# Optimization experiments

Hardware: AMD Instinct MI355X
Metric: run time of the kernel (lower is better)

Reference implementation:

```python
import jax, jax.numpy as jnp
import numpy as np

EMBED_TIME = 128
NUM_HEADS = 4
INPUT_DIM = 64
NHIDDEN = 256
B, LQ, LK = 4, 256, 512


def setup_inputs() -> dict:
    key = jax.random.key(0)
    ks = jax.random.split(key, 8)
    scale = np.float32(0.05)
    return {
        "query": jax.random.normal(ks[0], (B, LQ, EMBED_TIME), jnp.float32),
        "key_ts": jax.random.normal(ks[1], (B, LK, EMBED_TIME), jnp.float32),
        "value": jax.random.normal(ks[2], (B, LK, INPUT_DIM), jnp.float32),
        "mask": jax.random.randint(ks[3], (B, LK, INPUT_DIM), 0, 2, jnp.int32),
        # params stored [in, out] (transpose of torch nn.Linear convention)
        "Wq": jax.random.normal(ks[4], (EMBED_TIME, EMBED_TIME), jnp.float32) * scale,
        "bq": jnp.zeros((EMBED_TIME,), jnp.float32),
        "Wk": jax.random.normal(ks[5], (EMBED_TIME, EMBED_TIME), jnp.float32) * scale,
        "bk": jnp.zeros((EMBED_TIME,), jnp.float32),
        "W3": jax.random.normal(ks[6], (INPUT_DIM * NUM_HEADS, NHIDDEN), jnp.float32) * scale,
        "b3": jnp.zeros((NHIDDEN,), jnp.float32),
    }


def reference(query, key_ts, value, mask, Wq, bq, Wk, bk, W3, b3):
    b, lk, d = value.shape  # B, Lk, input_dim
    h = NUM_HEADS
    dk = EMBED_TIME // h
    # project & split heads: [B, L, E] -> [B, h, L, dk]
    q = (query @ Wq + bq).reshape(b, -1, h, dk).transpose(0, 2, 1, 3)
    k = (key_ts @ Wk + bk).reshape(b, -1, h, dk).transpose(0, 2, 1, 3)
    # scaled dot-product time scores: [B, h, Lq, Lk]
    scores = jnp.einsum('bhqe,bhke->bhqk', q, k) / np.float32(np.sqrt(dk))
    # broadcast scores over value feature dim, mask per feature: [B, h, Lq, Lk, D]
    scores = jnp.where(mask[:, None, None, :, :] == 0, jnp.float32(-1e9), scores[..., None])
    # softmax over key (time) axis, per feature
    p_attn = jax.nn.softmax(scores, axis=-2)
    # elementwise weighted reduce over Lk: [B, h, Lq, D]
    x = jnp.einsum('bhqkd,bkd->bhqd', p_attn, value)
    x = x.transpose(0, 2, 1, 3).reshape(b, -1, h * d)  # [B, Lq, h*D]
    # replicate reinitialize_dim: permute input columns of last layer by descending L1 norm
    perm = jnp.argsort(-jnp.sum(jnp.abs(W3), axis=1))
    return x @ W3[perm] + b3
```

## Files before the change

### kernel.cpp

```cpp
#include <hip/hip_runtime.h>
#include <math.h>

#define ETIME 128
#define NHEADS 4
#define DK 32
#define DIN 64
#define NHID 256
#define BB 4
#define LQg 256
#define LKg 512
#define KC 128
#define KCN 4
#define QT 16

__global__ __launch_bounds__(256) void proj_kernel(
    const float* __restrict__ query, const float* __restrict__ key_ts,
    const float* __restrict__ Wq, const float* __restrict__ bq,
    const float* __restrict__ Wk, const float* __restrict__ bk,
    float* __restrict__ qbuf, float* __restrict__ kbuf)
{
    __shared__ float in_lds[8][ETIME];
    const int t = threadIdx.x;
    const int r0 = blockIdx.x * 8;
    const bool is_q = (r0 < BB * LQg);
    const float* in   = is_q ? (query + (size_t)r0 * ETIME)
                             : (key_ts + (size_t)(r0 - BB * LQg) * ETIME);
    const float* W    = is_q ? Wq : Wk;
    const float* bias = is_q ? bq : bk;
    float* outp       = is_q ? (qbuf + (size_t)r0 * ETIME)
                             : (kbuf + (size_t)(r0 - BB * LQg) * ETIME);

    reinterpret_cast<float4*>(&in_lds[0][0])[t] =
        reinterpret_cast<const float4*>(in)[t];
    __syncthreads();

    const int j4 = t & 31;
    const int row = t >> 5;
    const float4* W4 = reinterpret_cast<const float4*>(W);
    float4 acc = make_float4(0.f, 0.f, 0.f, 0.f);
#pragma unroll 8
    for (int i = 0; i < ETIME; ++i) {
        const float4 w = W4[i * 32 + j4];
        const float xv = in_lds[row][i];
        acc.x = fmaf(xv, w.x, acc.x);
        acc.y = fmaf(xv, w.y, acc.y);
        acc.z = fmaf(xv, w.z, acc.z);
        acc.w = fmaf(xv, w.w, acc.w);
    }
    const float4 bb = reinterpret_cast<const float4*>(bias)[j4];
    acc.x += bb.x; acc.y += bb.y; acc.z += bb.z; acc.w += bb.w;
    reinterpret_cast<float4*>(outp + row * ETIME)[j4] = acc;
}

__global__ __launch_bounds__(256) void prep_kernel(
    const float* __restrict__ value, const int* __restrict__ mask,
    const float* __restrict__ W3,
    float2* __restrict__ vmbuf, float* __restrict__ sbuf)
{
    const int t = threadIdx.x;
    if (blockIdx.x < 256) {
        const int i = blockIdx.x * 256 + t;
        for (int idx = i; idx < BB * LKg * DIN; idx += 256 * 256) {
            const float mf = (float)mask[idx];
            vmbuf[idx] = make_float2(mf, value[idx] * mf);
        }
    } else {
        __shared__ float red[4];
        const int row = blockIdx.x - 256;
        float a = fabsf(W3[(size_t)row * NHID + t]);
#pragma unroll
        for (int off = 32; off; off >>= 1) a += __shfl_xor(a, off, 64);
        if ((t & 63) == 0) red[t >> 6] = a;
        __syncthreads();
        if (t == 0) sbuf[row] = red[0] + red[1] + red[2] + red[3];
    }
}

__global__ __launch_bounds__(NHID) void rank_kernel(
    const float* __restrict__ sbuf, int* __restrict__ perm)
{
    __shared__ float s[NHID];
    const int t = threadIdx.x;
    s[t] = sbuf[t];
    __syncthreads();
    const float si = s[t];
    int rank = 0;
#pragma unroll 8
    for (int j = 0; j < NHID; ++j) {
        const float sj = s[j];
        rank += (sj > si) || (sj == si && j < t);
    }
    perm[rank] = t;
}

__global__ __launch_bounds__(256, 4) void attn_chunk(
    const float* __restrict__ qbuf, const float* __restrict__ kbuf,
    const float2* __restrict__ vmbuf, float2* __restrict__ pbuf)
{
    __shared__ float qlds[QT][DK];
    __shared__ float klds[KC][DK + 1];
    __shared__ float S[QT][KC];

    const int t = threadIdx.x;
    int bid = blockIdx.x;
    bid = (bid & 7) * 128 + (bid >> 3);
    const int kc = bid & 3;
    const int qt = (bid >> 2) & 15;
    const int h  = (bid >> 6) & 3;
    const int b  = bid >> 8;
    const int qbase = qt * QT;
    const int kbase = kc * KC;

    for (int e = t; e < QT * DK; e += 256) {
        int q = e >> 5, i = e & 31;
        qlds[q][i] = qbuf[(size_t)(b * LQg + qbase + q) * ETIME + h * DK + i];
    }
    for (int e = t; e < KC * DK; e += 256) {
        int k = e >> 5, i = e & 31;
        klds[k][i] = kbuf[(size_t)(b * LKg + kbase + k) * ETIME + h * DK + i];
    }
    __syncthreads();

    {
        const int k = t & 127;
        const int qg = t >> 7;
        float acc[8] = {0, 0, 0, 0, 0, 0, 0, 0};
        for (int i = 0; i < DK; ++i) {
            float kv = klds[k][i];
#pragma unroll
            for (int jj = 0; jj < 8; ++jj)
                acc[jj] = fmaf(qlds[qg * 8 + jj][i], kv, acc[jj]);
        }
        const float rsq = 0.17677669529663687f;
#pragma unroll
        for (int jj = 0; jj < 8; ++jj)
            S[qg * 8 + jj][k] = __expf(acc[jj] * rsq);
    }
    __syncthreads();

    {
        const int d = t & 63;
        const int w = t >> 6;
        float num[4] = {0, 0, 0, 0}, den[4] = {0, 0, 0, 0};
        const float2* vp = vmbuf + (size_t)(b * LKg + kbase) * DIN + d;
#pragma unroll 4
        for (int k = 0; k < KC; ++k) {
            const float2 vm = vp[(size_t)k * DIN];
#pragma unroll
            for (int jj = 0; jj < 4; ++jj) {
                const float e = S[w * 4 + jj][k];
                num[jj] = fmaf(e, vm.y, num[jj]);
                den[jj] = fmaf(e, vm.x, den[jj]);
            }
        }
#pragma unroll
        for (int jj = 0; jj < 4; ++jj) {
            const int q = qbase + w * 4 + jj;
            pbuf[((size_t)((b * NHEADS + h) * LQg + q) * KCN + kc) * DIN + d] =
                make_float2(den[jj], num[jj]);
        }
    }
}

__global__ __launch_bounds__(256) void combine_kernel(
    const float2* __restrict__ pbuf, const int* __restrict__ perm,
    float* __restrict__ x2)
{
    const int t = threadIdx.x;
    const int bid = blockIdx.x;
    const int qt = bid & 15, h = (bid >> 4) & 3, b = bid >> 6;
    const int d = t & 63, w = t >> 6;
    const int pc = perm[h * DIN + d];
#pragma unroll
    for (int jj = 0; jj < 4; ++jj) {
        const int q = qt * QT + w * 4 + jj;
        const float2* pp = pbuf + ((size_t)((b * NHEADS + h) * LQg + q) * KCN) * DIN + d;
        float num = 0.f, den = 0.f;
#pragma unroll
        for (int kc = 0; kc < KCN; ++kc) {
            const float2 v = pp[kc * DIN];
            den += v.x; num += v.y;
        }
        x2[(size_t)(b * LQg + q) * NHID + pc] = num / den;
    }
}

__global__ __launch_bounds__(256) void out_kernel(
    const float* __restrict__ x2, const float* __restrict__ W3,
    const float* __restrict__ b3, float* __restrict__ out)
{
    __shared__ float x_lds[4][NHID];
    const int n = threadIdx.x;
    const int r0 = blockIdx.x * 4;
    reinterpret_cast<float4*>(&x_lds[0][0])[n] =
        reinterpret_cast<const float4*>(x2 + (size_t)r0 * NHID)[n];
    __syncthreads();

    float acc[4] = {0, 0, 0, 0};
#pragma unroll 8
    for (int c = 0; c < NHID; ++c) {
        const float w = W3[(size_t)c * NHID + n];
#pragma unroll
        for (int r = 0; r < 4; ++r) acc[r] = fmaf(x_lds[r][c], w, acc[r]);
    }
    const float bn = b3[n];
#pragma unroll
    for (int r = 0; r < 4; ++r) out[(size_t)(r0 + r) * NHID + n] = acc[r] + bn;
}

extern "C" void kernel_launch(void* const* d_in, const int* in_sizes, int n_in,
                              void* d_out, int out_size, void* d_ws, size_t ws_size,
                              hipStream_t stream) {
    const float* query  = (const float*)d_in[0];
    const float* key_ts = (const float*)d_in[1];
    const float* value  = (const float*)d_in[2];
    const int*   mask   = (const int*)d_in[3];
    const float* Wq     = (const float*)d_in[4];
    const float* bq     = (const float*)d_in[5];
    const float* Wk     = (const float*)d_in[6];
    const float* bk     = (const float*)d_in[7];
    const float* W3     = (const float*)d_in[8];
    const float* b3     = (const float*)d_in[9];
    float* out = (float*)d_out;

    char* ws = (char*)d_ws;
    float*  qbuf  = (float*) (ws);
    float*  kbuf  = (float*) (ws + (512u  << 10));
    float2* vmbuf = (float2*)(ws + (1536u << 10));
    float*  x2buf = (float*) (ws + (2560u << 10));
    float2* pbuf  = (float2*)(ws + (3584u << 10));
    int*    perm  = (int*)   (ws + (11776u << 10));
    float*  sbuf  = (float*) (ws + (11780u << 10));

    proj_kernel<<<384, 256, 0, stream>>>(query, key_ts, Wq, bq, Wk, bk, qbuf, kbuf);
    prep_kernel<<<512, 256, 0, stream>>>(value, mask, W3, vmbuf, sbuf);
    rank_kernel<<<1, NHID, 0, stream>>>(sbuf, perm);
    attn_chunk<<<BB * NHEADS * QT * KCN, 256, 0, stream>>>(qbuf, kbuf, vmbuf, pbuf);
    combine_kernel<<<BB * NHEADS * (LQg / QT), 256, 0, stream>>>(pbuf, perm, x2buf);
    out_kernel<<<BB * LQg / 4, 256, 0, stream>>>(x2buf, W3, b3, out);
}
```

Baseline: 56.97 us.

## Fuse prep, rank, combine and output kernels; vectorize attention loads

Merges projection, value/mask prep and W3 norm computation into one launch, and folds the rank computation and partial-sum combine into the output GEMM kernel, cutting the pipeline from six launches to three. The attention kernel now reads K rows directly into registers as float4, prescales Q, and uses float4 LDS reads in both inner loops. The cost is that every output block recomputes the 256-element rank and re-reads sbuf, and register pressure in the attention kernel goes up.

```diff
diff --git a/kernel.cpp b/kernel.cpp
--- a/kernel.cpp
+++ b/kernel.cpp
@@ -13,60 +13,58 @@
 #define KCN 4
 #define QT 16
 
-__global__ __launch_bounds__(256) void proj_kernel(
+__global__ __launch_bounds__(256) void prep_all(
     const float* __restrict__ query, const float* __restrict__ key_ts,
     const float* __restrict__ Wq, const float* __restrict__ bq,
     const float* __restrict__ Wk, const float* __restrict__ bk,
-    float* __restrict__ qbuf, float* __restrict__ kbuf)
+    const float* __restrict__ value, const int* __restrict__ mask,
+    const float* __restrict__ W3,
+    float* __restrict__ qbuf, float* __restrict__ kbuf,
+    float2* __restrict__ vmbuf, float* __restrict__ sbuf)
 {
     __shared__ float in_lds[8][ETIME];
+    __shared__ float red[4];
     const int t = threadIdx.x;
-    const int r0 = blockIdx.x * 8;
-    const bool is_q = (r0 < BB * LQg);
-    const float* in   = is_q ? (query + (size_t)r0 * ETIME)
-                             : (key_ts + (size_t)(r0 - BB * LQg) * ETIME);
-    const float* W    = is_q ? Wq : Wk;
-    const float* bias = is_q ? bq : bk;
-    float* outp       = is_q ? (qbuf + (size_t)r0 * ETIME)
-                             : (kbuf + (size_t)(r0 - BB * LQg) * ETIME);
-
-    reinterpret_cast<float4*>(&in_lds[0][0])[t] =
-        reinterpret_cast<const float4*>(in)[t];
-    __syncthreads();
-
-    const int j4 = t & 31;
-    const int row = t >> 5;
-    const float4* W4 = reinterpret_cast<const float4*>(W);
-    float4 acc = make_float4(0.f, 0.f, 0.f, 0.f);
+    const int blk = blockIdx.x;
+
+    if (blk < 384) {
+        const int r0 = blk * 8;
+        const bool is_q = (r0 < BB * LQg);
+        const float* in   = is_q ? (query + (size_t)r0 * ETIME)
+                                 : (key_ts + (size_t)(r0 - BB * LQg) * ETIME);
+        const float* W    = is_q ? Wq : Wk;
+        const float* bias = is_q ? bq : bk;
+        float* outp       = is_q ? (qbuf + (size_t)r0 * ETIME)
+                                 : (kbuf + (size_t)(r0 - BB * LQg) * ETIME);
+
+        reinterpret_cast<float4*>(&in_lds[0][0])[t] =
+            reinterpret_cast<const float4*>(in)[t];
+        __syncthreads();
+
+        const int j4 = t & 31;
+        const int row = t >> 5;
+        const float4* W4 = reinterpret_cast<const float4*>(W);
+        float4 acc = make_float4(0.f, 0.f, 0.f, 0.f);
 #pragma unroll 8
-    for (int i = 0; i < ETIME; ++i) {
-        const float4 w = W4[i * 32 + j4];
-        const float xv = in_lds[row][i];
-        acc.x = fmaf(xv, w.x, acc.x);
-        acc.y = fmaf(xv, w.y, acc.y);
-        acc.z = fmaf(xv, w.z, acc.z);
-        acc.w = fmaf(xv, w.w, acc.w);
-    }
-    const float4 bb = reinterpret_cast<const float4*>(bias)[j4];
-    acc.x += bb.x; acc.y += bb.y; acc.z += bb.z; acc.w += bb.w;
-    reinterpret_cast<float4*>(outp + row * ETIME)[j4] = acc;
-}
-
-__global__ __launch_bounds__(256) void prep_kernel(
-    const float* __restrict__ value, const int* __restrict__ mask,
-    const float* __restrict__ W3,
-    float2* __restrict__ vmbuf, float* __restrict__ sbuf)
-{
-    const int t = threadIdx.x;
-    if (blockIdx.x < 256) {
-        const int i = blockIdx.x * 256 + t;
+        for (int i = 0; i < ETIME; ++i) {
+            const float4 w = W4[i * 32 + j4];
+            const float xv = in_lds[row][i];
+            acc.x = fmaf(xv, w.x, acc.x);
+            acc.y = fmaf(xv, w.y, acc.y);
+            acc.z = fmaf(xv, w.z, acc.z);
+            acc.w = fmaf(xv, w.w, acc.w);
+        }
+        const float4 bb = reinterpret_cast<const float4*>(bias)[j4];
+        acc.x += bb.x; acc.y += bb.y; acc.z += bb.z; acc.w += bb.w;
+        reinterpret_cast<float4*>(outp + row * ETIME)[j4] = acc;
+    } else if (blk < 640) {
+        const int i = (blk - 384) * 256 + t;
         for (int idx = i; idx < BB * LKg * DIN; idx += 256 * 256) {
             const float mf = (float)mask[idx];
             vmbuf[idx] = make_float2(mf, value[idx] * mf);
         }
     } else {
-        __shared__ float red[4];
-        const int row = blockIdx.x - 256;
+        const int row = blk - 640;
         float a = fabsf(W3[(size_t)row * NHID + t]);
 #pragma unroll
         for (int off = 32; off; off >>= 1) a += __shfl_xor(a, off, 64);
@@ -74,23 +72,6 @@
         __syncthreads();
         if (t == 0) sbuf[row] = red[0] + red[1] + red[2] + red[3];
     }
-}
-
-__global__ __launch_bounds__(NHID) void rank_kernel(
-    const float* __restrict__ sbuf, int* __restrict__ perm)
-{
-    __shared__ float s[NHID];
-    const int t = threadIdx.x;
-    s[t] = sbuf[t];
-    __syncthreads();
-    const float si = s[t];
-    int rank = 0;
-#pragma unroll 8
-    for (int j = 0; j < NHID; ++j) {
-        const float sj = s[j];
-        rank += (sj > si) || (sj == si && j < t);
-    }
-    perm[rank] = t;
 }
 
 __global__ __launch_bounds__(256, 4) void attn_chunk(
@@ -98,7 +79,6 @@
     const float2* __restrict__ vmbuf, float2* __restrict__ pbuf)
 {
     __shared__ float qlds[QT][DK];
-    __shared__ float klds[KC][DK + 1];
     __shared__ float S[QT][KC];
 
     const int t = threadIdx.x;
@@ -111,30 +91,41 @@
     const int qbase = qt * QT;
     const int kbase = kc * KC;
 
-    for (int e = t; e < QT * DK; e += 256) {
-        int q = e >> 5, i = e & 31;
-        qlds[q][i] = qbuf[(size_t)(b * LQg + qbase + q) * ETIME + h * DK + i];
-    }
-    for (int e = t; e < KC * DK; e += 256) {
-        int k = e >> 5, i = e & 31;
-        klds[k][i] = kbuf[(size_t)(b * LKg + kbase + k) * ETIME + h * DK + i];
+    if (t < 128) {
+        const int q = t >> 3, j = t & 7;
+        float4 v = reinterpret_cast<const float4*>(
+            qbuf + (size_t)(b * LQg + qbase + q) * ETIME + h * DK)[j];
+        const float rsq = 0.17677669529663687f;
+        v.x *= rsq; v.y *= rsq; v.z *= rsq; v.w *= rsq;
+        reinterpret_cast<float4*>(&qlds[q][0])[j] = v;
     }
     __syncthreads();
 
     {
         const int k = t & 127;
         const int qg = t >> 7;
+        const float* krow = kbuf + (size_t)(b * LKg + kbase + k) * ETIME + h * DK;
+        float4 kr[8];
+#pragma unroll
+        for (int i = 0; i < 8; ++i)
+            kr[i] = reinterpret_cast<const float4*>(krow)[i];
         float acc[8] = {0, 0, 0, 0, 0, 0, 0, 0};
-        for (int i = 0; i < DK; ++i) {
-            float kv = klds[k][i];
-#pragma unroll
-            for (int jj = 0; jj < 8; ++jj)
-                acc[jj] = fmaf(qlds[qg * 8 + jj][i], kv, acc[jj]);
-        }
-        const float rsq = 0.17677669529663687f;
+#pragma unroll
+        for (int i4 = 0; i4 < 8; ++i4) {
+            const float4 kv = kr[i4];
+#pragma unroll
+            for (int jj = 0; jj < 8; ++jj) {
+                const float4 qv =
+                    reinterpret_cast<const float4*>(&qlds[qg * 8 + jj][0])[i4];
+                acc[jj] = fmaf(qv.x, kv.x, acc[jj]);
+                acc[jj] = fmaf(qv.y, kv.y, acc[jj]);
+                acc[jj] = fmaf(qv.z, kv.z, acc[jj]);
+                acc[jj] = fmaf(qv.w, kv.w, acc[jj]);
+            }
+        }
 #pragma unroll
         for (int jj = 0; jj < 8; ++jj)
-            S[qg * 8 + jj][k] = __expf(acc[jj] * rsq);
+            S[qg * 8 + jj][k] = __expf(acc[jj]);
     }
     __syncthreads();
 
@@ -144,13 +135,18 @@
         float num[4] = {0, 0, 0, 0}, den[4] = {0, 0, 0, 0};
         const float2* vp = vmbuf + (size_t)(b * LKg + kbase) * DIN + d;
 #pragma unroll 4
-        for (int k = 0; k < KC; ++k) {
-            const float2 vm = vp[(size_t)k * DIN];
+        for (int k4 = 0; k4 < KC / 4; ++k4) {
+            float2 vm[4];
+#pragma unroll
+            for (int u = 0; u < 4; ++u) vm[u] = vp[(size_t)(k4 * 4 + u) * DIN];
 #pragma unroll
             for (int jj = 0; jj < 4; ++jj) {
-                const float e = S[w * 4 + jj][k];
-                num[jj] = fmaf(e, vm.y, num[jj]);
-                den[jj] = fmaf(e, vm.x, den[jj]);
+                const float4 e4 =
+                    reinterpret_cast<const float4*>(&S[w * 4 + jj][0])[k4];
+                num[jj] = fmaf(e4.x, vm[0].y, num[jj]); den[jj] = fmaf(e4.x, vm[0].x, den[jj]);
+                num[jj] = fmaf(e4.y, vm[1].y, num[jj]); den[jj] = fmaf(e4.y, vm[1].x, den[jj]);
+                num[jj] = fmaf(e4.z, vm[2].y, num[jj]); den[jj] = fmaf(e4.z, vm[2].x, den[jj]);
+                num[jj] = fmaf(e4.w, vm[3].y, num[jj]); den[jj] = fmaf(e4.w, vm[3].x, den[jj]);
             }
         }
 #pragma unroll
@@ -162,50 +158,65 @@
     }
 }
 
-__global__ __launch_bounds__(256) void combine_kernel(
-    const float2* __restrict__ pbuf, const int* __restrict__ perm,
-    float* __restrict__ x2)
+__global__ __launch_bounds__(256) void out_fused(
+    const float2* __restrict__ pbuf, const float* __restrict__ W3,
+    const float* __restrict__ b3, const float* __restrict__ sbuf,
+    float* __restrict__ out)
 {
+    __shared__ float s_lds[NHID];
+    __shared__ float xraw[4][NHID];
+    __shared__ float x2[4][NHID];
     const int t = threadIdx.x;
-    const int bid = blockIdx.x;
-    const int qt = bid & 15, h = (bid >> 4) & 3, b = bid >> 6;
-    const int d = t & 63, w = t >> 6;
-    const int pc = perm[h * DIN + d];
-#pragma unroll
-    for (int jj = 0; jj < 4; ++jj) {
-        const int q = qt * QT + w * 4 + jj;
-        const float2* pp = pbuf + ((size_t)((b * NHEADS + h) * LQg + q) * KCN) * DIN + d;
+    const int r0 = blockIdx.x * 4;
+    const int b = r0 >> 8;
+    const int q0 = r0 & 255;
+    const int h = t >> 6, d = t & 63;
+
+    s_lds[t] = sbuf[t];
+#pragma unroll
+    for (int r = 0; r < 4; ++r) {
+        const float2* pp =
+            pbuf + ((size_t)((b * NHEADS + h) * LQg + q0 + r) * KCN) * DIN + d;
         float num = 0.f, den = 0.f;
 #pragma unroll
         for (int kc = 0; kc < KCN; ++kc) {
             const float2 v = pp[kc * DIN];
             den += v.x; num += v.y;
         }
-        x2[(size_t)(b * LQg + q) * NHID + pc] = num / den;
-    }
-}
-
-__global__ __launch_bounds__(256) void out_kernel(
-    const float* __restrict__ x2, const float* __restrict__ W3,
-    const float* __restrict__ b3, float* __restrict__ out)
-{
-    __shared__ float x_lds[4][NHID];
-    const int n = threadIdx.x;
-    const int r0 = blockIdx.x * 4;
-    reinterpret_cast<float4*>(&x_lds[0][0])[n] =
-        reinterpret_cast<const float4*>(x2 + (size_t)r0 * NHID)[n];
+        xraw[r][t] = num / den;
+    }
+    __syncthreads();
+
+    const float si = s_lds[t];
+    int rank = 0;
+#pragma unroll 8
+    for (int j = 0; j < NHID; ++j) {
+        const float sj = s_lds[j];
+        rank += (sj > si) || (sj == si && j < t);
+    }
+#pragma unroll
+    for (int r = 0; r < 4; ++r) x2[r][t] = xraw[r][rank];
     __syncthreads();
 
     float acc[4] = {0, 0, 0, 0};
-#pragma unroll 8
-    for (int c = 0; c < NHID; ++c) {
-        const float w = W3[(size_t)c * NHID + n];
-#pragma unroll
-        for (int r = 0; r < 4; ++r) acc[r] = fmaf(x_lds[r][c], w, acc[r]);
-    }
-    const float bn = b3[n];
-#pragma unroll
-    for (int r = 0; r < 4; ++r) out[(size_t)(r0 + r) * NHID + n] = acc[r] + bn;
+#pragma unroll 4
+    for (int c4 = 0; c4 < NHID / 4; ++c4) {
+        const float w0 = W3[(size_t)(c4 * 4 + 0) * NHID + t];
+        const float w1 = W3[(size_t)(c4 * 4 + 1) * NHID + t];
+        const float w2 = W3[(size_t)(c4 * 4 + 2) * NHID + t];
+        const float w3 = W3[(size_t)(c4 * 4 + 3) * NHID + t];
+#pragma unroll
+        for (int r = 0; r < 4; ++r) {
+            const float4 xv = reinterpret_cast<const float4*>(&x2[r][0])[c4];
+            acc[r] = fmaf(xv.x, w0, acc[r]);
+            acc[r] = fmaf(xv.y, w1, acc[r]);
+            acc[r] = fmaf(xv.z, w2, acc[r]);
+            acc[r] = fmaf(xv.w, w3, acc[r]);
+        }
+    }
+    const float bn = b3[t];
+#pragma unroll
+    for (int r = 0; r < 4; ++r) out[(size_t)(r0 + r) * NHID + t] = acc[r] + bn;
 }
 
 extern "C" void kernel_launch(void* const* d_in, const int* in_sizes, int n_in,
@@ -227,15 +238,11 @@
     float*  qbuf  = (float*) (ws);
     float*  kbuf  = (float*) (ws + (512u  << 10));
     float2* vmbuf = (float2*)(ws + (1536u << 10));
-    float*  x2buf = (float*) (ws + (2560u << 10));
-    float2* pbuf  = (float2*)(ws + (3584u << 10));
-    int*    perm  = (int*)   (ws + (11776u << 10));
-    float*  sbuf  = (float*) (ws + (11780u << 10));
-
-    proj_kernel<<<384, 256, 0, stream>>>(query, key_ts, Wq, bq, Wk, bk, qbuf, kbuf);
-    prep_kernel<<<512, 256, 0, stream>>>(value, mask, W3, vmbuf, sbuf);
-    rank_kernel<<<1, NHID, 0, stream>>>(sbuf, perm);
+    float2* pbuf  = (float2*)(ws + (2560u << 10));
+    float*  sbuf  = (float*) (ws + (10752u << 10));
+
+    prep_all<<<896, 256, 0, stream>>>(query, key_ts, Wq, bq, Wk, bk,
+                                      value, mask, W3, qbuf, kbuf, vmbuf, sbuf);
     attn_chunk<<<BB * NHEADS * QT * KCN, 256, 0, stream>>>(qbuf, kbuf, vmbuf, pbuf);
-    combine_kernel<<<BB * NHEADS * (LQg / QT), 256, 0, stream>>>(pbuf, perm, x2buf);
-    out_kernel<<<BB * LQg / 4, 256, 0, stream>>>(x2buf, W3, b3, out);
-}
+    out_fused<<<BB * LQg / 4, 256, 0, stream>>>(pbuf, W3, b3, sbuf, out);
+}
```

After: 51.43 us. 1.11x faster.
